# Kernel tuning notes

Hardware: AMD Instinct MI355X
Metric: run time of the kernel (lower is better)

Reference implementation:

```python
import jax, jax.numpy as jnp
import numpy as np

N_NODES = 10000
N_EDGES = 160000
N_GRAPHS = 64
D_IN = 128
D_H = 512
N_CLS = 2
L = 3
EPS = 1e-7   # GENConv message eps / clamp min
MAXV = 10.0  # GENConv power-mean clamp max
BN_EPS = 1e-5


def setup_inputs() -> dict:
    key = jax.random.key(0)
    ks = jax.random.split(key, 8)
    return {
        "x": jax.random.normal(ks[0], (N_NODES, D_IN), jnp.float32),
        "W0": jax.random.normal(ks[1], (D_IN, D_H), jnp.float32) * 0.05,
        "Wrest": jax.random.normal(ks[2], (L - 1, D_H, D_H), jnp.float32) * 0.05,
        "bconv": jnp.zeros((L, D_H), jnp.float32),
        "p": jnp.ones((L,), jnp.float32),
        "msg_scale": jnp.ones((L,), jnp.float32),
        "bn_gamma": jnp.ones((L, D_H), jnp.float32),
        "bn_beta": jnp.zeros((L, D_H), jnp.float32),
        "fc1_W": jax.random.normal(ks[3], (2 * D_H, D_H), jnp.float32) * 0.05,
        "fc1_b": jnp.zeros((D_H,), jnp.float32),
        "bn4_g": jnp.ones((D_H,), jnp.float32),
        "bn4_b": jnp.zeros((D_H,), jnp.float32),
        "fc2_W": jax.random.normal(ks[4], (D_H, N_CLS), jnp.float32) * 0.05,
        "fc2_b": jnp.zeros((N_CLS,), jnp.float32),
        "edge_index": jax.random.randint(ks[5], (2, N_EDGES), 0, N_NODES, dtype=jnp.int32),
        "batch": jnp.sort(jax.random.randint(ks[6], (N_NODES,), 0, N_GRAPHS, dtype=jnp.int32)),
    }


def _batchnorm(h, g, b):
    # training-mode BatchNorm1d: batch statistics, biased variance
    mu = h.mean(axis=0)
    var = ((h - mu) ** 2).mean(axis=0)
    return (h - mu) * jax.lax.rsqrt(var + BN_EPS) * g + b


def _genconv(x, W, b, p, scale, src, dst):
    # message: m_e = relu(x_src) + eps  (no edge_attr), clamped to [eps, 10]
    m = jnp.minimum(jax.nn.relu(x[src]) + EPS, MAXV)          # [E, d]
    # power-mean aggregation onto target nodes
    deg = jax.ops.segment_sum(jnp.ones((src.shape[0],), x.dtype), dst, N_NODES)
    agg = jax.ops.segment_sum(m ** p, dst, N_NODES) / jnp.maximum(deg, 1.0)[:, None]
    agg = jnp.clip(agg, EPS, MAXV) ** (1.0 / p)               # [N, d]
    # MessageNorm: l2-normalize aggregated message, rescale by ||x|| * scale
    msg = agg / jnp.maximum(jnp.linalg.norm(agg, axis=-1, keepdims=True), 1e-12)
    xn = jnp.linalg.norm(x, axis=-1, keepdims=True)
    out = x + msg * xn * scale                                # residual add
    return out @ W + b                                        # 1-layer MLP


def reference(x, W0, Wrest, bconv, p, msg_scale, bn_gamma, bn_beta,
              fc1_W, fc1_b, bn4_g, bn4_b, fc2_W, fc2_b, edge_index, batch):
    src, dst = edge_index[0], edge_index[1]
    h = x
    jk = None
    for i in range(L):
        W = W0 if i == 0 else Wrest[i - 1]
        h = _genconv(h, W, bconv[i], p[i], msg_scale[i], src, dst)
        h = jax.nn.relu(_batchnorm(h, bn_gamma[i], bn_beta[i]))
        jk = h if jk is None else jnp.maximum(jk, h)          # JumpingKnowledge 'max'
    # global max + mean pooling per graph
    cnt = jax.ops.segment_sum(jnp.ones((N_NODES,), h.dtype), batch, N_GRAPHS)
    gmean = jax.ops.segment_sum(jk, batch, N_GRAPHS) / jnp.maximum(cnt, 1.0)[:, None]
    gmax = jax.ops.segment_max(jk, batch, N_GRAPHS)
    gmax = jnp.where(cnt[:, None] > 0, gmax, 0.0)
    g = jnp.concatenate([gmax, gmean], axis=1)                # [G, 1024]
    g = jax.nn.relu(_batchnorm(g @ fc1_W + fc1_b, bn4_g, bn4_b))
    # dropout: eval mode (identity)
    return g @ fc2_W + fc2_b                                  # [G, num_classes]
```

## Files before the change

kernel.cpp:

```cpp
#include <hip/hip_runtime.h>
#include <hip/hip_bf16.h>
#include <math.h>

#define N_NODES 10000
#define N_GRAPHS 64
#define N_EDGES 160000
#define D_INPUT 128
#define D_H 512
#define EPS 1e-7f
#define MAXV 10.0f
#define BN_EPS 1e-5f
#define M_PAD 10112

typedef __attribute__((ext_vector_type(4))) float f32x4;
typedef __attribute__((ext_vector_type(8))) __bf16 bf16x8;

__global__ __launch_bounds__(256) void hist_kernel(const int* __restrict__ dst,
                                                   int* __restrict__ cnt) {
  int i = blockIdx.x * blockDim.x + threadIdx.x;
  if (i < N_EDGES) atomicAdd(&cnt[dst[i]], 1);
}

__global__ __launch_bounds__(256) void scan_kernel(int* __restrict__ cnt,
                                                   int* __restrict__ rowptr) {
  __shared__ int ps[256];
  int tid = threadIdx.x;
  const int CH = (N_NODES + 255) / 256;
  int b0 = tid * CH;
  int b1 = min(N_NODES, b0 + CH);
  int s = 0;
  for (int i = b0; i < b1; i++) s += cnt[i];
  ps[tid] = s;
  __syncthreads();
  for (int off = 1; off < 256; off <<= 1) {
    int v = (tid >= off) ? ps[tid - off] : 0;
    __syncthreads();
    ps[tid] += v;
    __syncthreads();
  }
  int run = (tid == 0) ? 0 : ps[tid - 1];
  for (int i = b0; i < b1; i++) {
    rowptr[i] = run;
    run += cnt[i];
    cnt[i] = 0;
  }
  if (tid == 255) rowptr[N_NODES] = run;
}

__global__ __launch_bounds__(256) void scatter_kernel(
    const int* __restrict__ src, const int* __restrict__ dst,
    const int* __restrict__ rowptr, int* __restrict__ cursor,
    int* __restrict__ csr_src) {
  int i = blockIdx.x * blockDim.x + threadIdx.x;
  if (i < N_EDGES) {
    int t = dst[i];
    int pos = rowptr[t] + atomicAdd(&cursor[t], 1);
    csr_src[pos] = src[i];
  }
}

__global__ __launch_bounds__(512) void bn_affine(float* __restrict__ stats,
                                                 const float* __restrict__ gamma,
                                                 const float* __restrict__ beta,
                                                 float* __restrict__ aff) {
  int c = threadIdx.x;
  const float invN = 1.0f / (float)N_NODES;
  float mean = stats[c] * invN;
  float var = stats[D_H + c] * invN - mean * mean;
  float sc = rsqrtf(var + BN_EPS) * gamma[c];
  aff[c] = sc;
  aff[D_H + c] = beta[c] - mean * sc;
  stats[c] = 0.f;
  stats[D_H + c] = 0.f;
}

__global__ __launch_bounds__(256) void msg0_kernel(const float* __restrict__ x,
                                                   const float* __restrict__ p_ptr,
                                                   __hip_bfloat16* __restrict__ msgb) {
  float p = *p_ptr;
  bool p1 = (p == 1.0f);
  const int total = N_NODES * D_INPUT / 2;
  for (int i = blockIdx.x * 256 + threadIdx.x; i < total; i += gridDim.x * 256) {
    float2 v = ((const float2*)x)[i];
    float m0 = fminf(fmaxf(v.x, 0.f) + EPS, MAXV);
    float m1 = fminf(fmaxf(v.y, 0.f) + EPS, MAXV);
    if (!p1) { m0 = powf(m0, p); m1 = powf(m1, p); }
    __hip_bfloat162 o;
    o.x = __float2bfloat16(m0);
    o.y = __float2bfloat16(m1);
    ((__hip_bfloat162*)msgb)[i] = o;
  }
}

template <int D, bool BN>
__global__ __launch_bounds__(256) void agg_msgnorm_kernel(
    const float* __restrict__ h, const float* __restrict__ aff,
    const __hip_bfloat16* __restrict__ msgb,
    const int* __restrict__ rowptr, const int* __restrict__ csr_src,
    const float* __restrict__ p_ptr, const float* __restrict__ scale_ptr,
    __hip_bfloat16* __restrict__ out) {
  constexpr int C = D / 2;
  constexpr int SL = 256 / C;
  int n = blockIdx.x;
  int tid = threadIdx.x;
  int col = tid % C;
  int slice = tid / C;
  int lo = rowptr[n], hi = rowptr[n + 1];
  float p = *p_ptr;
  float scale = *scale_ptr;
  bool p1 = (p == 1.0f);
  float invp = 1.0f / p;
  float inv_dg = 1.0f / fmaxf((float)(hi - lo), 1.0f);
  const float2* h2 = (const float2*)h;
  const uint* mg = (const uint*)msgb;

  __shared__ int s_src[256];
  float accx = 0.f, accy = 0.f;
  for (int base = lo; base < hi; base += 256) {
    int m = min(256, hi - base);
    __syncthreads();
    if (tid < m) s_src[tid] = csr_src[base + tid];
    __syncthreads();
    int j = slice;
    for (; j + 3 * SL < m; j += 4 * SL) {
      int s0 = s_src[j], s1 = s_src[j + SL], s2 = s_src[j + 2 * SL], s3 = s_src[j + 3 * SL];
      uint u0 = mg[(size_t)s0 * C + col];
      uint u1 = mg[(size_t)s1 * C + col];
      uint u2 = mg[(size_t)s2 * C + col];
      uint u3 = mg[(size_t)s3 * C + col];
      accx += (__uint_as_float(u0 << 16) + __uint_as_float(u1 << 16)) +
              (__uint_as_float(u2 << 16) + __uint_as_float(u3 << 16));
      accy += (__uint_as_float(u0 & 0xFFFF0000u) + __uint_as_float(u1 & 0xFFFF0000u)) +
              (__uint_as_float(u2 & 0xFFFF0000u) + __uint_as_float(u3 & 0xFFFF0000u));
    }
    for (; j < m; j += SL) {
      uint u = mg[(size_t)s_src[j] * C + col];
      accx += __uint_as_float(u << 16);
      accy += __uint_as_float(u & 0xFFFF0000u);
    }
  }

  if constexpr (SL > 1) {
    __shared__ float sacc[2][256];
    sacc[0][tid] = accx;
    sacc[1][tid] = accy;
    __syncthreads();
    if (tid < C) {
#pragma unroll
      for (int s = 1; s < SL; s++) {
        accx += sacc[0][s * C + tid];
        accy += sacc[1][s * C + tid];
      }
    }
  }

  float a0 = 0.f, a1 = 0.f, hv0 = 0.f, hv1 = 0.f, sa = 0.f, sh = 0.f;
  if (tid < C) {
    a0 = fminf(fmaxf(accx * inv_dg, EPS), MAXV);
    a1 = fminf(fmaxf(accy * inv_dg, EPS), MAXV);
    if (!p1) { a0 = powf(a0, invp); a1 = powf(a1, invp); }
    float2 hx = h2[(size_t)n * C + tid];
    if constexpr (BN) {
      float2 s2 = ((const float2*)aff)[tid];
      float2 b2 = ((const float2*)(aff + D_H))[tid];
      hx.x = fmaxf(hx.x * s2.x + b2.x, 0.f);
      hx.y = fmaxf(hx.y * s2.y + b2.y, 0.f);
    }
    hv0 = hx.x;
    hv1 = hx.y;
    sa = a0 * a0 + a1 * a1;
    sh = hv0 * hv0 + hv1 * hv1;
  }
  for (int off = 32; off; off >>= 1) {
    sa += __shfl_down(sa, off);
    sh += __shfl_down(sh, off);
  }
  __shared__ float red[2][4];
  __shared__ float tot[2];
  int wid = tid >> 6;
  if ((tid & 63) == 0) { red[0][wid] = sa; red[1][wid] = sh; }
  __syncthreads();
  if (tid == 0) {
    tot[0] = red[0][0] + red[0][1] + red[0][2] + red[0][3];
    tot[1] = red[1][0] + red[1][1] + red[1][2] + red[1][3];
  }
  __syncthreads();
  float k = sqrtf(tot[1]) * scale / fmaxf(sqrtf(tot[0]), 1e-12f);
  if (tid < C) {
    __hip_bfloat162 o2;
    o2.x = __float2bfloat16(hv0 + a0 * k);
    o2.y = __float2bfloat16(hv1 + a1 * k);
    ((__hip_bfloat162*)out)[(size_t)n * C + tid] = o2;
  }
}

__global__ __launch_bounds__(256) void convert_wt(const float* __restrict__ W,
                                                  __hip_bfloat16* __restrict__ Wt,
                                                  int K, int N) {
  __shared__ float tile[32][33];
  int k0 = blockIdx.x * 32, n0 = blockIdx.y * 32;
  int tx = threadIdx.x & 31, ty = threadIdx.x >> 5;
  for (int i = ty; i < 32; i += 8)
    tile[i][tx] = W[(size_t)(k0 + i) * N + n0 + tx];
  __syncthreads();
  for (int i = ty; i < 32; i += 8)
    Wt[(size_t)(n0 + i) * K + k0 + tx] = __float2bfloat16(tile[tx][i]);
}

__global__ __launch_bounds__(256) void mfma_gemm(
    const __hip_bfloat16* __restrict__ A, const __hip_bfloat16* __restrict__ Bt,
    const float* __restrict__ bias, float* __restrict__ C, float* __restrict__ stats,
    int M, int K) {
  __shared__ ushort As[128 * 64];
  __shared__ ushort Bs[128 * 64];
  __shared__ float sred[128][2];
  int tid = threadIdx.x;
  int l = tid & 63;
  int w = tid >> 6;
  int wm = w >> 1, wn = w & 1;
  int row0 = blockIdx.x * 128;
  int col0 = blockIdx.y * 128;

  f32x4 acc[4][4];
#pragma unroll
  for (int m = 0; m < 4; m++)
#pragma unroll
    for (int n = 0; n < 4; n++) acc[m][n] = (f32x4){0.f, 0.f, 0.f, 0.f};

  const ushort* Ag = (const ushort*)A;
  const ushort* Bg = (const ushort*)Bt;
  char* AsB = (char*)As;
  char* BsB = (char*)Bs;

  if (tid < 128) { sred[tid][0] = 0.f; sred[tid][1] = 0.f; }

  int srow = tid >> 3;
  int scb = (tid & 7) * 16;
  int wbyte = scb ^ ((srow & 7) << 4);
  int scol = scb >> 1;

  int lswz = (l & 7) << 4;
  int kb = (l >> 4) * 16;
  int arow = wm * 64 + (l & 15);
  int brow = wn * 64 + (l & 15);

  for (int k0 = 0; k0 < K; k0 += 64) {
    uint4 ra[4], rb[4];
#pragma unroll
    for (int j = 0; j < 4; j++) {
      int row = j * 32 + srow;
      ra[j] = *(const uint4*)(Ag + (size_t)(row0 + row) * K + k0 + scol);
      rb[j] = *(const uint4*)(Bg + (size_t)(col0 + row) * K + k0 + scol);
    }
#pragma unroll
    for (int j = 0; j < 4; j++) {
      int row = j * 32 + srow;
      *(uint4*)(AsB + row * 128 + wbyte) = ra[j];
      *(uint4*)(BsB + row * 128 + wbyte) = rb[j];
    }
    __syncthreads();
#pragma unroll
    for (int kk = 0; kk < 2; kk++) {
      bf16x8 af[4], bfr[4];
#pragma unroll
      for (int m = 0; m < 4; m++)
        af[m] = *(const bf16x8*)(AsB + (arow + m * 16) * 128 + ((kk * 64 + kb) ^ lswz));
#pragma unroll
      for (int n = 0; n < 4; n++)
        bfr[n] = *(const bf16x8*)(BsB + (brow + n * 16) * 128 + ((kk * 64 + kb) ^ lswz));
#pragma unroll
      for (int m = 0; m < 4; m++)
#pragma unroll
        for (int n = 0; n < 4; n++)
          acc[m][n] = __builtin_amdgcn_mfma_f32_16x16x32_bf16(af[m], bfr[n], acc[m][n], 0, 0, 0);
    }
    __syncthreads();
  }

  int crow0 = row0 + wm * 64 + (l >> 4) * 4;
  int ccol0 = col0 + wn * 64 + (l & 15);
#pragma unroll
  for (int n = 0; n < 4; n++) {
    int col = ccol0 + n * 16;
    float bv = bias[col];
    float ps = 0.f, pq = 0.f;
#pragma unroll
    for (int m = 0; m < 4; m++) {
#pragma unroll
      for (int r = 0; r < 4; r++) {
        int rr = crow0 + m * 16 + r;
        if (rr < M) {
          float v = acc[m][n][r] + bv;
          C[(size_t)rr * D_H + col] = v;
          ps += v;
          pq += v * v;
        }
      }
    }
    ps += __shfl_down(ps, 16); pq += __shfl_down(pq, 16);
    ps += __shfl_down(ps, 32); pq += __shfl_down(pq, 32);
    if ((l >> 4) == 0) {
      atomicAdd(&sred[wn * 64 + n * 16 + (l & 15)][0], ps);
      atomicAdd(&sred[wn * 64 + n * 16 + (l & 15)][1], pq);
    }
  }
  __syncthreads();
  if (tid < 128) {
    atomicAdd(&stats[col0 + tid], sred[tid][0]);
    atomicAdd(&stats[D_H + col0 + tid], sred[tid][1]);
  }
}

template <bool WRITE_MSG>
__global__ __launch_bounds__(256) void jk_msg_update(
    const float* __restrict__ hlin, const float* __restrict__ aff,
    float* __restrict__ jk, const float* __restrict__ p_ptr,
    __hip_bfloat16* __restrict__ msgb, int layer) {
  float p = 1.f;
  bool p1 = true;
  if constexpr (WRITE_MSG) {
    p = *p_ptr;
    p1 = (p == 1.0f);
  }
  const int total = N_NODES * D_H / 4;
  for (int idx = blockIdx.x * blockDim.x + threadIdx.x; idx < total;
       idx += gridDim.x * blockDim.x) {
    int c4 = idx & 127;
    float4 x = ((const float4*)hlin)[idx];
    float4 sc = ((const float4*)aff)[c4];
    float4 sh = ((const float4*)(aff + D_H))[c4];
    float4 v;
    v.x = fmaxf(x.x * sc.x + sh.x, 0.f);
    v.y = fmaxf(x.y * sc.y + sh.y, 0.f);
    v.z = fmaxf(x.z * sc.z + sh.z, 0.f);
    v.w = fmaxf(x.w * sc.w + sh.w, 0.f);
    if constexpr (WRITE_MSG) {
      float m0 = fminf(v.x + EPS, MAXV);
      float m1 = fminf(v.y + EPS, MAXV);
      float m2 = fminf(v.z + EPS, MAXV);
      float m3 = fminf(v.w + EPS, MAXV);
      if (!p1) { m0 = powf(m0, p); m1 = powf(m1, p); m2 = powf(m2, p); m3 = powf(m3, p); }
      __hip_bfloat162 o01, o23;
      o01.x = __float2bfloat16(m0); o01.y = __float2bfloat16(m1);
      o23.x = __float2bfloat16(m2); o23.y = __float2bfloat16(m3);
      ((__hip_bfloat162*)msgb)[2 * idx] = o01;
      ((__hip_bfloat162*)msgb)[2 * idx + 1] = o23;
    }
    if (layer != 0) {
      float4 j = ((const float4*)jk)[idx];
      v.x = fmaxf(v.x, j.x);
      v.y = fmaxf(v.y, j.y);
      v.z = fmaxf(v.z, j.z);
      v.w = fmaxf(v.w, j.w);
    }
    ((float4*)jk)[idx] = v;
  }
}

__device__ __forceinline__ int lower_bound_i(const int* a, int n, int v) {
  int lo = 0, hi = n;
  while (lo < hi) {
    int mid = (lo + hi) >> 1;
    if (a[mid] < v) lo = mid + 1; else hi = mid;
  }
  return lo;
}

__global__ __launch_bounds__(256) void pool_kernel(const float* __restrict__ jk,
                                                   const int* __restrict__ batch,
                                                   float* __restrict__ g) {
  int gid = blockIdx.x;
  int col = blockIdx.y * 64 + (threadIdx.x & 63);
  int slice = threadIdx.x >> 6;
  int lo = lower_bound_i(batch, N_NODES, gid);
  int hi = lower_bound_i(batch, N_NODES, gid + 1);
  float mx = 0.f, sm = 0.f;
  int r = lo + slice;
  for (; r + 12 < hi; r += 16) {
    float v0 = jk[(size_t)r * D_H + col];
    float v1 = jk[(size_t)(r + 4) * D_H + col];
    float v2 = jk[(size_t)(r + 8) * D_H + col];
    float v3 = jk[(size_t)(r + 12) * D_H + col];
    mx = fmaxf(fmaxf(fmaxf(mx, v0), fmaxf(v1, v2)), v3);
    sm += (v0 + v1) + (v2 + v3);
  }
  for (; r < hi; r += 4) {
    float v = jk[(size_t)r * D_H + col];
    mx = fmaxf(mx, v);
    sm += v;
  }
  __shared__ float smax[4][64];
  __shared__ float ssum[4][64];
  smax[slice][threadIdx.x & 63] = mx;
  ssum[slice][threadIdx.x & 63] = sm;
  __syncthreads();
  if (slice == 0) {
    int c = threadIdx.x & 63;
    mx = fmaxf(fmaxf(smax[0][c], smax[1][c]), fmaxf(smax[2][c], smax[3][c]));
    sm = ssum[0][c] + ssum[1][c] + ssum[2][c] + ssum[3][c];
    float inv_cnt = 1.0f / fmaxf((float)(hi - lo), 1.0f);
    g[(size_t)gid * 1024 + col] = (hi > lo) ? mx : 0.f;
    g[(size_t)gid * 1024 + D_H + col] = sm * inv_cnt;
  }
}

__global__ __launch_bounds__(256) void fc1_kernel(const float* __restrict__ g,
                                                  const float* __restrict__ W,
                                                  const float* __restrict__ b,
                                                  float* __restrict__ out) {
  __shared__ float sg[1024];
  __shared__ float sred[4][64];
  int gid = blockIdx.x;
  int tid = threadIdx.x;
  ((float4*)sg)[tid] = ((const float4*)(g + (size_t)gid * 1024))[tid];
  __syncthreads();
  int cl = tid & 63;
  int slice = tid >> 6;
  int col = blockIdx.y * 64 + cl;
  int k0 = slice * 256;
  float acc = 0.f;
#pragma unroll 4
  for (int k = k0; k < k0 + 256; k++) acc += sg[k] * W[(size_t)k * D_H + col];
  sred[slice][cl] = acc;
  __syncthreads();
  if (slice == 0)
    out[(size_t)gid * D_H + col] =
        sred[0][cl] + sred[1][cl] + sred[2][cl] + sred[3][cl] + b[col];
}

__global__ __launch_bounds__(256) void bn4_kernel(const float* __restrict__ x,
                                                  const float* __restrict__ gmm,
                                                  const float* __restrict__ bb,
                                                  float* __restrict__ y) {
  int cl = threadIdx.x & 63;
  int slice = threadIdx.x >> 6;
  int c = blockIdx.x * 64 + cl;
  float s = 0.f, q = 0.f;
#pragma unroll
  for (int r = slice * 16; r < slice * 16 + 16; r++) {
    float v = x[(size_t)r * D_H + c];
    s += v; q += v * v;
  }
  __shared__ float ss[4][64], sq[4][64];
  ss[slice][cl] = s;
  sq[slice][cl] = q;
  __syncthreads();
  float S = ss[0][cl] + ss[1][cl] + ss[2][cl] + ss[3][cl];
  float Q = sq[0][cl] + sq[1][cl] + sq[2][cl] + sq[3][cl];
  float mean = S * (1.0f / N_GRAPHS);
  float var = Q * (1.0f / N_GRAPHS) - mean * mean;
  float rs = rsqrtf(var + BN_EPS) * gmm[c];
  float sh = bb[c] - mean * rs;
#pragma unroll
  for (int r = slice * 16; r < slice * 16 + 16; r++)
    y[(size_t)r * D_H + c] = fmaxf(x[(size_t)r * D_H + c] * rs + sh, 0.f);
}

__global__ __launch_bounds__(64) void fc2_kernel(const float* __restrict__ y,
                                                 const float* __restrict__ W,
                                                 const float* __restrict__ b,
                                                 float* __restrict__ out) {
  int gid = blockIdx.x;
  int lane = threadIdx.x;
  float a0 = 0.f, a1 = 0.f;
  for (int k = lane; k < D_H; k += 64) {
    float v = y[(size_t)gid * D_H + k];
    a0 += v * W[k * 2 + 0];
    a1 += v * W[k * 2 + 1];
  }
  for (int off = 32; off; off >>= 1) {
    a0 += __shfl_down(a0, off);
    a1 += __shfl_down(a1, off);
  }
  if (lane == 0) {
    out[gid * 2 + 0] = a0 + b[0];
    out[gid * 2 + 1] = a1 + b[1];
  }
}

extern "C" void kernel_launch(void* const* d_in, const int* in_sizes, int n_in,
                              void* d_out, int out_size, void* d_ws, size_t ws_size,
                              hipStream_t stream) {
  const float* x       = (const float*)d_in[0];
  const float* W0      = (const float*)d_in[1];
  const float* Wrest   = (const float*)d_in[2];
  const float* bconv   = (const float*)d_in[3];
  const float* p       = (const float*)d_in[4];
  const float* mscale  = (const float*)d_in[5];
  const float* bn_g    = (const float*)d_in[6];
  const float* bn_b    = (const float*)d_in[7];
  const float* fc1_W   = (const float*)d_in[8];
  const float* fc1_b   = (const float*)d_in[9];
  const float* bn4_g   = (const float*)d_in[10];
  const float* bn4_b   = (const float*)d_in[11];
  const float* fc2_W   = (const float*)d_in[12];
  const float* fc2_b   = (const float*)d_in[13];
  const int*   eidx    = (const int*)d_in[14];
  const int*   batch   = (const int*)d_in[15];
  float* out = (float*)d_out;

  const int* src = eidx;
  const int* dst = eidx + N_EDGES;

  float* ws = (float*)d_ws;
  const size_t NH = (size_t)N_NODES * D_H;
  float* hlin  = ws;
  float* jk    = hlin + NH;
  float* stats = jk + NH;
  float* aff   = stats + 1024;
  __hip_bfloat16* residb = (__hip_bfloat16*)(aff + 1024);
  __hip_bfloat16* msgb = residb + (size_t)M_PAD * D_H;
  __hip_bfloat16* w0t = msgb + NH;
  __hip_bfloat16* w1t = w0t + 512 * 128;
  __hip_bfloat16* w2t = w1t + 512 * 512;
  int* cnt     = (int*)(w2t + 512 * 512);
  int* rowptr  = cnt + N_NODES;
  int* csr_src = rowptr + N_NODES + 1;
  float* g     = (float*)(csr_src + N_EDGES);
  float* g2lin = g + 64 * 1024;
  float* g2    = g2lin + 64 * D_H;

  convert_wt<<<dim3(D_INPUT / 32, D_H / 32), 256, 0, stream>>>(W0, w0t, D_INPUT, D_H);
  convert_wt<<<dim3(D_H / 32, D_H / 32), 256, 0, stream>>>(Wrest, w1t, D_H, D_H);
  convert_wt<<<dim3(D_H / 32, D_H / 32), 256, 0, stream>>>(Wrest + (size_t)D_H * D_H, w2t, D_H, D_H);

  hipMemsetAsync(cnt, 0, N_NODES * sizeof(int), stream);
  hist_kernel<<<(N_EDGES + 255) / 256, 256, 0, stream>>>(dst, cnt);
  scan_kernel<<<1, 256, 0, stream>>>(cnt, rowptr);
  scatter_kernel<<<(N_EDGES + 255) / 256, 256, 0, stream>>>(src, dst, rowptr, cnt, csr_src);

  hipMemsetAsync(stats, 0, 1024 * sizeof(float), stream);
  msg0_kernel<<<1280, 256, 0, stream>>>(x, p, msgb);

  for (int layer = 0; layer < 3; layer++) {
    if (layer == 0)
      agg_msgnorm_kernel<D_INPUT, false><<<N_NODES, 256, 0, stream>>>(
          x, nullptr, msgb, rowptr, csr_src, p + layer, mscale + layer, residb);
    else
      agg_msgnorm_kernel<D_H, true><<<N_NODES, 256, 0, stream>>>(
          hlin, aff, msgb, rowptr, csr_src, p + layer, mscale + layer, residb);
    const __hip_bfloat16* Wt = (layer == 0) ? w0t : (layer == 1 ? w1t : w2t);
    int K = (layer == 0) ? D_INPUT : D_H;
    mfma_gemm<<<dim3(M_PAD / 128, D_H / 128), 256, 0, stream>>>(
        residb, Wt, bconv + (size_t)layer * D_H, hlin, stats, N_NODES, K);
    bn_affine<<<1, 512, 0, stream>>>(stats, bn_g + (size_t)layer * D_H,
                                     bn_b + (size_t)layer * D_H, aff);
    if (layer < 2)
      jk_msg_update<true><<<2048, 256, 0, stream>>>(hlin, aff, jk, p + layer + 1, msgb, layer);
    else
      jk_msg_update<false><<<2048, 256, 0, stream>>>(hlin, aff, jk, nullptr, nullptr, layer);
  }

  pool_kernel<<<dim3(N_GRAPHS, 8), 256, 0, stream>>>(jk, batch, g);
  fc1_kernel<<<dim3(N_GRAPHS, 8), 256, 0, stream>>>(g, fc1_W, fc1_b, g2lin);
  bn4_kernel<<<8, 256, 0, stream>>>(g2lin, bn4_g, bn4_b, g2);
  fc2_kernel<<<N_GRAPHS, 64, 0, stream>>>(g2, fc2_W, fc2_b, out);
}
```

Baseline: 286.6 us.

## Vectorize aggregation and pooling loads, merge setup kernels and memsets

The aggregation kernel now has each thread gather 16-byte chunks (8 bf16 features) per neighbour instead of 4 bytes, with a shared-memory reduction across slices. The pooling kernel is likewise switched to float4 loads over 16 row slices. The scan kernel loads and stores its counts with int4, and the three weight-conversion launches plus two memsets are folded into one launch. The aim is fewer memory transactions in the gather-bound aggregation and less launch overhead. The cost is more registers per thread and fewer threads sharing each node's edge list.

```diff
diff --git a/kernel.cpp b/kernel.cpp
--- a/kernel.cpp
+++ b/kernel.cpp
@@ -15,6 +15,9 @@
 typedef __attribute__((ext_vector_type(4))) float f32x4;
 typedef __attribute__((ext_vector_type(8))) __bf16 bf16x8;
 
+__device__ __forceinline__ float bf_lo(uint u) { return __uint_as_float(u << 16); }
+__device__ __forceinline__ float bf_hi(uint u) { return __uint_as_float(u & 0xFFFF0000u); }
+
 __global__ __launch_bounds__(256) void hist_kernel(const int* __restrict__ dst,
                                                    int* __restrict__ cnt) {
   int i = blockIdx.x * blockDim.x + threadIdx.x;
@@ -25,26 +28,42 @@
                                                    int* __restrict__ rowptr) {
   __shared__ int ps[256];
   int tid = threadIdx.x;
-  const int CH = (N_NODES + 255) / 256;
+  const int CH = 40;
   int b0 = tid * CH;
-  int b1 = min(N_NODES, b0 + CH);
+  bool active = (b0 < N_NODES);
+  int v[CH];
   int s = 0;
-  for (int i = b0; i < b1; i++) s += cnt[i];
+  if (active) {
+    const int4* c4p = (const int4*)(cnt + b0);
+#pragma unroll
+    for (int i = 0; i < CH / 4; i++) {
+      int4 q = c4p[i];
+      v[4 * i] = q.x; v[4 * i + 1] = q.y; v[4 * i + 2] = q.z; v[4 * i + 3] = q.w;
+      s += q.x + q.y + q.z + q.w;
+    }
+  }
   ps[tid] = s;
   __syncthreads();
   for (int off = 1; off < 256; off <<= 1) {
-    int v = (tid >= off) ? ps[tid - off] : 0;
+    int t = (tid >= off) ? ps[tid - off] : 0;
     __syncthreads();
-    ps[tid] += v;
+    ps[tid] += t;
     __syncthreads();
   }
   int run = (tid == 0) ? 0 : ps[tid - 1];
-  for (int i = b0; i < b1; i++) {
-    rowptr[i] = run;
-    run += cnt[i];
-    cnt[i] = 0;
-  }
-  if (tid == 255) rowptr[N_NODES] = run;
+  if (active) {
+    int r[CH];
+#pragma unroll
+    for (int i = 0; i < CH; i++) { r[i] = run; run += v[i]; }
+    int4* rp = (int4*)(rowptr + b0);
+    int4* cz = (int4*)(cnt + b0);
+#pragma unroll
+    for (int i = 0; i < CH / 4; i++) {
+      rp[i] = make_int4(r[4 * i], r[4 * i + 1], r[4 * i + 2], r[4 * i + 3]);
+      cz[i] = make_int4(0, 0, 0, 0);
+    }
+  }
+  if (tid == 255) rowptr[N_NODES] = ps[255];
 }
 
 __global__ __launch_bounds__(256) void scatter_kernel(
@@ -99,23 +118,31 @@
     const int* __restrict__ rowptr, const int* __restrict__ csr_src,
     const float* __restrict__ p_ptr, const float* __restrict__ scale_ptr,
     __hip_bfloat16* __restrict__ out) {
-  constexpr int C = D / 2;
-  constexpr int SL = 256 / C;
+  constexpr int C4 = D / 8;
+  constexpr int SL = 256 / C4;
   int n = blockIdx.x;
   int tid = threadIdx.x;
-  int col = tid % C;
-  int slice = tid / C;
+  int col = tid & (C4 - 1);
+  int slice = tid / C4;
   int lo = rowptr[n], hi = rowptr[n + 1];
   float p = *p_ptr;
   float scale = *scale_ptr;
   bool p1 = (p == 1.0f);
   float invp = 1.0f / p;
   float inv_dg = 1.0f / fmaxf((float)(hi - lo), 1.0f);
-  const float2* h2 = (const float2*)h;
-  const uint* mg = (const uint*)msgb;
+  const uint4* mg = (const uint4*)msgb;
 
   __shared__ int s_src[256];
-  float accx = 0.f, accy = 0.f;
+  float acc[8] = {0.f, 0.f, 0.f, 0.f, 0.f, 0.f, 0.f, 0.f};
+
+#define ACCU(U)                                   \
+  do {                                            \
+    acc[0] += bf_lo((U).x); acc[1] += bf_hi((U).x); \
+    acc[2] += bf_lo((U).y); acc[3] += bf_hi((U).y); \
+    acc[4] += bf_lo((U).z); acc[5] += bf_hi((U).z); \
+    acc[6] += bf_lo((U).w); acc[7] += bf_hi((U).w); \
+  } while (0)
+
   for (int base = lo; base < hi; base += 256) {
     int m = min(256, hi - base);
     __syncthreads();
@@ -123,53 +150,57 @@
     __syncthreads();
     int j = slice;
     for (; j + 3 * SL < m; j += 4 * SL) {
-      int s0 = s_src[j], s1 = s_src[j + SL], s2 = s_src[j + 2 * SL], s3 = s_src[j + 3 * SL];
-      uint u0 = mg[(size_t)s0 * C + col];
-      uint u1 = mg[(size_t)s1 * C + col];
-      uint u2 = mg[(size_t)s2 * C + col];
-      uint u3 = mg[(size_t)s3 * C + col];
-      accx += (__uint_as_float(u0 << 16) + __uint_as_float(u1 << 16)) +
-              (__uint_as_float(u2 << 16) + __uint_as_float(u3 << 16));
-      accy += (__uint_as_float(u0 & 0xFFFF0000u) + __uint_as_float(u1 & 0xFFFF0000u)) +
-              (__uint_as_float(u2 & 0xFFFF0000u) + __uint_as_float(u3 & 0xFFFF0000u));
+      uint4 u0 = mg[(size_t)s_src[j] * C4 + col];
+      uint4 u1 = mg[(size_t)s_src[j + SL] * C4 + col];
+      uint4 u2 = mg[(size_t)s_src[j + 2 * SL] * C4 + col];
+      uint4 u3 = mg[(size_t)s_src[j + 3 * SL] * C4 + col];
+      ACCU(u0); ACCU(u1); ACCU(u2); ACCU(u3);
     }
     for (; j < m; j += SL) {
-      uint u = mg[(size_t)s_src[j] * C + col];
-      accx += __uint_as_float(u << 16);
-      accy += __uint_as_float(u & 0xFFFF0000u);
-    }
-  }
-
-  if constexpr (SL > 1) {
-    __shared__ float sacc[2][256];
-    sacc[0][tid] = accx;
-    sacc[1][tid] = accy;
-    __syncthreads();
-    if (tid < C) {
-#pragma unroll
-      for (int s = 1; s < SL; s++) {
-        accx += sacc[0][s * C + tid];
-        accy += sacc[1][s * C + tid];
-      }
-    }
-  }
-
-  float a0 = 0.f, a1 = 0.f, hv0 = 0.f, hv1 = 0.f, sa = 0.f, sh = 0.f;
-  if (tid < C) {
-    a0 = fminf(fmaxf(accx * inv_dg, EPS), MAXV);
-    a1 = fminf(fmaxf(accy * inv_dg, EPS), MAXV);
-    if (!p1) { a0 = powf(a0, invp); a1 = powf(a1, invp); }
-    float2 hx = h2[(size_t)n * C + tid];
+      uint4 u = mg[(size_t)s_src[j] * C4 + col];
+      ACCU(u);
+    }
+  }
+#undef ACCU
+
+  __shared__ float sacc[256][9];
+#pragma unroll
+  for (int i = 0; i < 8; i++) sacc[tid][i] = acc[i];
+  __syncthreads();
+
+  float a[8], hv[8];
+  float sa = 0.f, sh = 0.f;
+  if (tid < C4) {
+#pragma unroll
+    for (int s = 1; s < SL; s++)
+#pragma unroll
+      for (int i = 0; i < 8; i++) acc[i] += sacc[s * C4 + tid][i];
+#pragma unroll
+    for (int i = 0; i < 8; i++) {
+      float v = fminf(fmaxf(acc[i] * inv_dg, EPS), MAXV);
+      if (!p1) v = powf(v, invp);
+      a[i] = v;
+      sa += v * v;
+    }
+    const float4* hrow = (const float4*)(h + (size_t)n * D) + tid * 2;
+    float4 h0 = hrow[0], h1 = hrow[1];
+    hv[0] = h0.x; hv[1] = h0.y; hv[2] = h0.z; hv[3] = h0.w;
+    hv[4] = h1.x; hv[5] = h1.y; hv[6] = h1.z; hv[7] = h1.w;
     if constexpr (BN) {
-      float2 s2 = ((const float2*)aff)[tid];
-      float2 b2 = ((const float2*)(aff + D_H))[tid];
-      hx.x = fmaxf(hx.x * s2.x + b2.x, 0.f);
-      hx.y = fmaxf(hx.y * s2.y + b2.y, 0.f);
-    }
-    hv0 = hx.x;
-    hv1 = hx.y;
-    sa = a0 * a0 + a1 * a1;
-    sh = hv0 * hv0 + hv1 * hv1;
+      const float4* sc4 = (const float4*)aff + tid * 2;
+      const float4* sh4 = (const float4*)(aff + D_H) + tid * 2;
+      float4 s0 = sc4[0], s1 = sc4[1], b0 = sh4[0], b1 = sh4[1];
+      hv[0] = fmaxf(hv[0] * s0.x + b0.x, 0.f);
+      hv[1] = fmaxf(hv[1] * s0.y + b0.y, 0.f);
+      hv[2] = fmaxf(hv[2] * s0.z + b0.z, 0.f);
+      hv[3] = fmaxf(hv[3] * s0.w + b0.w, 0.f);
+      hv[4] = fmaxf(hv[4] * s1.x + b1.x, 0.f);
+      hv[5] = fmaxf(hv[5] * s1.y + b1.y, 0.f);
+      hv[6] = fmaxf(hv[6] * s1.z + b1.z, 0.f);
+      hv[7] = fmaxf(hv[7] * s1.w + b1.w, 0.f);
+    }
+#pragma unroll
+    for (int i = 0; i < 8; i++) sh += hv[i] * hv[i];
   }
   for (int off = 32; off; off >>= 1) {
     sa += __shfl_down(sa, off);
@@ -186,22 +217,44 @@
   }
   __syncthreads();
   float k = sqrtf(tot[1]) * scale / fmaxf(sqrtf(tot[0]), 1e-12f);
-  if (tid < C) {
-    __hip_bfloat162 o2;
-    o2.x = __float2bfloat16(hv0 + a0 * k);
-    o2.y = __float2bfloat16(hv1 + a1 * k);
-    ((__hip_bfloat162*)out)[(size_t)n * C + tid] = o2;
-  }
-}
-
-__global__ __launch_bounds__(256) void convert_wt(const float* __restrict__ W,
-                                                  __hip_bfloat16* __restrict__ Wt,
-                                                  int K, int N) {
+  if (tid < C4) {
+    alignas(16) __hip_bfloat162 o[4];
+#pragma unroll
+    for (int i = 0; i < 4; i++) {
+      o[i].x = __float2bfloat16(hv[2 * i] + a[2 * i] * k);
+      o[i].y = __float2bfloat16(hv[2 * i + 1] + a[2 * i + 1] * k);
+    }
+    ((uint4*)(out + (size_t)n * D))[tid] = *(const uint4*)o;
+  }
+}
+
+__global__ __launch_bounds__(256) void convert_all(
+    const float* __restrict__ W0, const float* __restrict__ Wrest,
+    __hip_bfloat16* __restrict__ w0t, __hip_bfloat16* __restrict__ w1t,
+    __hip_bfloat16* __restrict__ w2t, int* __restrict__ cnt,
+    float* __restrict__ stats) {
+  int z = blockIdx.z;
+  const float* W;
+  __hip_bfloat16* Wt;
+  int K;
+  if (z == 0) { W = W0; Wt = w0t; K = D_INPUT; }
+  else if (z == 1) { W = Wrest; Wt = w1t; K = D_H; }
+  else { W = Wrest + (size_t)D_H * D_H; Wt = w2t; K = D_H; }
+
+  if (z == 0 && blockIdx.x >= 4) {
+    int bid = (blockIdx.x - 4) * 16 + blockIdx.y;
+    int idx = bid * 256 + threadIdx.x;
+    if (idx < N_NODES) cnt[idx] = 0;
+    int sidx = idx - N_NODES;
+    if (sidx >= 0 && sidx < 1024) stats[sidx] = 0.f;
+    return;
+  }
+
   __shared__ float tile[32][33];
   int k0 = blockIdx.x * 32, n0 = blockIdx.y * 32;
   int tx = threadIdx.x & 31, ty = threadIdx.x >> 5;
   for (int i = ty; i < 32; i += 8)
-    tile[i][tx] = W[(size_t)(k0 + i) * N + n0 + tx];
+    tile[i][tx] = W[(size_t)(k0 + i) * D_H + n0 + tx];
   __syncthreads();
   for (int i = ty; i < 32; i += 8)
     Wt[(size_t)(n0 + i) * K + k0 + tx] = __float2bfloat16(tile[tx][i]);
@@ -370,37 +423,49 @@
                                                    const int* __restrict__ batch,
                                                    float* __restrict__ g) {
   int gid = blockIdx.x;
-  int col = blockIdx.y * 64 + (threadIdx.x & 63);
-  int slice = threadIdx.x >> 6;
+  int cl = threadIdx.x & 15;
+  int slice = threadIdx.x >> 4;
+  int f4c = blockIdx.y * 16 + cl;
   int lo = lower_bound_i(batch, N_NODES, gid);
   int hi = lower_bound_i(batch, N_NODES, gid + 1);
-  float mx = 0.f, sm = 0.f;
+  const float4* J = (const float4*)jk;
+  float4 mx = make_float4(0.f, 0.f, 0.f, 0.f);
+  float4 sm = make_float4(0.f, 0.f, 0.f, 0.f);
   int r = lo + slice;
-  for (; r + 12 < hi; r += 16) {
-    float v0 = jk[(size_t)r * D_H + col];
-    float v1 = jk[(size_t)(r + 4) * D_H + col];
-    float v2 = jk[(size_t)(r + 8) * D_H + col];
-    float v3 = jk[(size_t)(r + 12) * D_H + col];
-    mx = fmaxf(fmaxf(fmaxf(mx, v0), fmaxf(v1, v2)), v3);
-    sm += (v0 + v1) + (v2 + v3);
-  }
-  for (; r < hi; r += 4) {
-    float v = jk[(size_t)r * D_H + col];
-    mx = fmaxf(mx, v);
-    sm += v;
-  }
-  __shared__ float smax[4][64];
-  __shared__ float ssum[4][64];
-  smax[slice][threadIdx.x & 63] = mx;
-  ssum[slice][threadIdx.x & 63] = sm;
+  for (; r + 16 < hi; r += 32) {
+    float4 v0 = J[(size_t)r * 128 + f4c];
+    float4 v1 = J[(size_t)(r + 16) * 128 + f4c];
+    mx.x = fmaxf(fmaxf(mx.x, v0.x), v1.x);
+    mx.y = fmaxf(fmaxf(mx.y, v0.y), v1.y);
+    mx.z = fmaxf(fmaxf(mx.z, v0.z), v1.z);
+    mx.w = fmaxf(fmaxf(mx.w, v0.w), v1.w);
+    sm.x += v0.x + v1.x; sm.y += v0.y + v1.y;
+    sm.z += v0.z + v1.z; sm.w += v0.w + v1.w;
+  }
+  for (; r < hi; r += 16) {
+    float4 v = J[(size_t)r * 128 + f4c];
+    mx.x = fmaxf(mx.x, v.x); mx.y = fmaxf(mx.y, v.y);
+    mx.z = fmaxf(mx.z, v.z); mx.w = fmaxf(mx.w, v.w);
+    sm.x += v.x; sm.y += v.y; sm.z += v.z; sm.w += v.w;
+  }
+  __shared__ float4 smax[16][16];
+  __shared__ float4 ssum[16][16];
+  smax[slice][cl] = mx;
+  ssum[slice][cl] = sm;
   __syncthreads();
   if (slice == 0) {
-    int c = threadIdx.x & 63;
-    mx = fmaxf(fmaxf(smax[0][c], smax[1][c]), fmaxf(smax[2][c], smax[3][c]));
-    sm = ssum[0][c] + ssum[1][c] + ssum[2][c] + ssum[3][c];
-    float inv_cnt = 1.0f / fmaxf((float)(hi - lo), 1.0f);
-    g[(size_t)gid * 1024 + col] = (hi > lo) ? mx : 0.f;
-    g[(size_t)gid * 1024 + D_H + col] = sm * inv_cnt;
+#pragma unroll
+    for (int s = 1; s < 16; s++) {
+      float4 m2 = smax[s][cl], s2 = ssum[s][cl];
+      mx.x = fmaxf(mx.x, m2.x); mx.y = fmaxf(mx.y, m2.y);
+      mx.z = fmaxf(mx.z, m2.z); mx.w = fmaxf(mx.w, m2.w);
+      sm.x += s2.x; sm.y += s2.y; sm.z += s2.z; sm.w += s2.w;
+    }
+    float ic = 1.0f / fmaxf((float)(hi - lo), 1.0f);
+    if (hi <= lo) mx = make_float4(0.f, 0.f, 0.f, 0.f);
+    sm.x *= ic; sm.y *= ic; sm.z *= ic; sm.w *= ic;
+    ((float4*)(g + (size_t)gid * 1024))[f4c] = mx;
+    ((float4*)(g + (size_t)gid * 1024 + D_H))[f4c] = sm;
   }
 }
 
@@ -520,16 +585,12 @@
   float* g2lin = g + 64 * 1024;
   float* g2    = g2lin + 64 * D_H;
 
-  convert_wt<<<dim3(D_INPUT / 32, D_H / 32), 256, 0, stream>>>(W0, w0t, D_INPUT, D_H);
-  convert_wt<<<dim3(D_H / 32, D_H / 32), 256, 0, stream>>>(Wrest, w1t, D_H, D_H);
-  convert_wt<<<dim3(D_H / 32, D_H / 32), 256, 0, stream>>>(Wrest + (size_t)D_H * D_H, w2t, D_H, D_H);
-
-  hipMemsetAsync(cnt, 0, N_NODES * sizeof(int), stream);
+  convert_all<<<dim3(16, 16, 3), 256, 0, stream>>>(W0, Wrest, w0t, w1t, w2t, cnt, stats);
+
   hist_kernel<<<(N_EDGES + 255) / 256, 256, 0, stream>>>(dst, cnt);
   scan_kernel<<<1, 256, 0, stream>>>(cnt, rowptr);
   scatter_kernel<<<(N_EDGES + 255) / 256, 256, 0, stream>>>(src, dst, rowptr, cnt, csr_src);
 
-  hipMemsetAsync(stats, 0, 1024 * sizeof(float), stream);
   msg0_kernel<<<1280, 256, 0, stream>>>(x, p, msgb);
 
   for (int layer = 0; layer < 3; layer++) {
```

Result: faster. 279.1 us (-2.6%).
